# Kernel optimization log

Hardware: AMD Instinct MI355X
Metric: run time of the kernel (lower is better)

The kernel has to match this reference:

```python
import jax, jax.numpy as jnp
import numpy as np

LN_EPS = 1e-5
NRM_EPS = 1e-12


def layernorm(x, w, b):
    mu = x.mean(-1, keepdims=True)
    var = ((x - mu) ** 2).mean(-1, keepdims=True)
    return (x - mu) * jax.lax.rsqrt(var + LN_EPS) * w + b


def cdist(x, y):
    # Euclidean pairwise distance over trailing (N, C): (..., N, C) x (..., M, C) -> (..., N, M)
    x2 = (x * x).sum(-1)
    y2 = (y * y).sum(-1)
    xy = jnp.einsum('...ic,...jc->...ij', x, y)
    return jnp.sqrt(jnp.maximum(x2[..., :, None] + y2[..., None, :] - 2.0 * xy, NRM_EPS))


def l2norm_last(x):
    n = jnp.sqrt((x * x).sum(-1, keepdims=True))
    return x / jnp.maximum(n, NRM_EPS)


def attn_qcs_sd(anchor, positive, neg1, neg2, k, alpha):
    # anchor/positive: (B,N,C); neg1/neg2: (2,B,N,C)
    # torch.tensor(neg) in the original detaches neg1/neg2 from autograd
    neg1 = jax.lax.stop_gradient(neg1)
    neg2 = jax.lax.stop_gradient(neg2)
    k = k + 1.0
    S_p = cdist(positive, anchor)           # (B,N,N)
    S_p = S_p - S_p.min()
    S_p = S_p.max() - S_p
    S_a = l2norm_last(S_p).sum(1)           # (B,N)
    S_p1 = l2norm_last(jnp.swapaxes(S_p, 1, 2)).sum(1)  # (B,N)

    def proc(D):  # (B,N,N) -> (B,N)
        D = D - D.min()
        return l2norm_last(D).sum(1)

    def pair(neg, tgt):  # neg (2,B,N,C), tgt (B,N,C)
        D = cdist(neg, jnp.broadcast_to(tgt[None], neg.shape))  # (2,B,N,N)
        return proc(D[0]), proc(D[1])

    d11, d12 = pair(neg1, anchor)
    d21, d22 = pair(neg2, anchor)
    map1 = S_a + k * ((d11 + d12) / 2 * alpha + (1 - alpha) * ((d21 + d22) / 2))
    d11, d12 = pair(neg1, positive)
    d21, d22 = pair(neg2, positive)
    map2 = S_p1 + k * ((d11 + d12) / 2 * alpha + (1 - alpha) * ((d21 + d22) / 2))
    return map1[..., None], map2[..., None]  # (B,N,1) each


def setup_inputs() -> dict:
    key = jax.random.key(0)
    B, N, C = 8, 1024, 768
    ks = jax.random.split(key, 12)
    s = 1.0 / np.sqrt(C)
    sh = 1.0 / np.sqrt(4 * C)
    return {
        'anchor': jax.random.normal(ks[0], (B, N, C), jnp.float32),
        'positive': jax.random.normal(ks[1], (B, N, C), jnp.float32),
        'neg1': jax.random.normal(ks[2], (2, B, N, C), jnp.float32),
        'neg2': jax.random.normal(ks[3], (2, B, N, C), jnp.float32),
        'norm1_w': jnp.ones((C,), jnp.float32),
        'norm1_b': jnp.zeros((C,), jnp.float32),
        'norm2_w': jnp.ones((C,), jnp.float32),
        'norm2_b': jnp.zeros((C,), jnp.float32),
        'proj_W': jax.random.uniform(ks[4], (C, 2 * C), jnp.float32, -s, s),
        'proj_b': jax.random.uniform(ks[5], (2 * C,), jnp.float32, -s, s),
        'fc1_W': jax.random.uniform(ks[6], (C, 4 * C), jnp.float32, -s, s),
        'fc1_b': jax.random.uniform(ks[7], (4 * C,), jnp.float32, -s, s),
        'fc2_W': jax.random.uniform(ks[8], (4 * C, C), jnp.float32, -sh, sh),
        'fc2_b': jax.random.uniform(ks[9], (C,), jnp.float32, -sh, sh),
        'theta': jnp.float32(0.0),
        'alpha': jnp.float32(0.0),
    }


def reference(anchor, positive, neg1, neg2, norm1_w, norm1_b, norm2_w, norm2_b,
              proj_W, proj_b, fc1_W, fc1_b, fc2_W, fc2_b, theta, alpha):
    def projsplit(x):
        y = x @ proj_W + proj_b
        C = x.shape[-1]
        return y[..., :C], y[..., C:]  # qk, v

    anc = layernorm(anchor, norm1_w, norm1_b)
    pos = layernorm(positive, norm1_w, norm1_b)
    n1 = layernorm(neg1, norm1_w, norm1_b)   # (2,B,N,C)
    n2 = layernorm(neg2, norm1_w, norm1_b)
    qk_x, v_x = projsplit(anc)
    qk_p, v_p = projsplit(pos)
    qk_n1, v_n1 = projsplit(n1)
    qk_n2, v_n2 = projsplit(n2)

    k = jnp.tanh(theta)
    al = jax.nn.sigmoid(alpha)

    a_a, a_p = attn_qcs_sd(qk_x, qk_p, qk_n1, qk_n2, k, al)
    n1_a, n1_p = attn_qcs_sd(qk_n1[0], qk_n1[1], jnp.stack([qk_x, qk_p]), qk_n2, k, al)
    n2_a, n2_p = attn_qcs_sd(qk_n2[0], qk_n2[1], jnp.stack([qk_x, qk_p]), qk_n1, k, al)

    anc_o = a_a * v_x + anc
    pos_o = a_p * v_p + pos
    neg1_o = jnp.stack([n1_a * v_n1[0] * n1[0], n1_p * v_n1[1] * n1[1]])
    neg2_o = jnp.stack([n2_a * v_n2[0] * n2[0], n2_p * v_n2[1] * n2[1]])

    def block(x):
        h = layernorm(x, norm2_w, norm2_b)
        h = jax.nn.gelu(h @ fc1_W + fc1_b, approximate=False) @ fc2_W + fc2_b
        return h + x

    return block(anc_o), block(pos_o), block(neg1_o), block(neg2_o)
```

## Files before the change

kernel.cpp:

```cpp
#include <hip/hip_runtime.h>
#include <hip/hip_bf16.h>


typedef short bshort8 __attribute__((ext_vector_type(8)));
typedef unsigned short u16x8 __attribute__((ext_vector_type(8)));
typedef float f32x4  __attribute__((ext_vector_type(4)));

#define AS1 __attribute__((address_space(1)))
#define AS3 __attribute__((address_space(3)))

#define B_   8
#define N_   1024
#define C_   768
#define MT   8192
#define M6   49152

#define OFF_QKNORM   0ull
#define OFF_MAPS     196608ull
#define OFF_STATS    393216ull
#define OFF_WBUF     2359296ull
#define OFF_MM       3342336ull
#define MEMSET_BYTES 3342464ull
#define OFF_WTPROJ   3342592ull
#define OFF_WTFC1    5701888ull
#define OFF_WTFC2    10420480ull
#define OFF_LNBF     15139072ull
#define OFF_QKBF     90636544ull
#define OFF_XHBF     OFF_QKBF
#define OFF_VBF      166134016ull
#define OFF_DBUF     241631488ull
#define OFF_H1BF     OFF_DBUF

__constant__ int cSU[15] = {1,3,5, 2,3,4,5, 2,3,4,5, 4,5,4,5};
__constant__ int cSV[15] = {0,2,4, 0,0,0,0, 1,1,1,1, 2,2,3,3};
__constant__ int cTA[15] = {0,0,0, 1,1,2,2, 1,1,2,2, 2,2,2,2};
__constant__ int cTB[15] = {0,0,0, 1,1,1,1, 1,1,1,1, 2,2,2,2};

__device__ __forceinline__ void gll16(const void* g, void* l) {
    __builtin_amdgcn_global_load_lds((const AS1 unsigned int*)g,
                                     (AS3 unsigned int*)l, 16, 0, 0);
}
__device__ __forceinline__ unsigned short f2bu(float v) {
    __hip_bfloat16 h = __float2bfloat16(v);
    return *reinterpret_cast<unsigned short*>(&h);
}
__device__ __forceinline__ float bu2f(unsigned short u) {
    __hip_bfloat16 h;
    *reinterpret_cast<unsigned short*>(&h) = u;
    return __bfloat162float(h);
}
__device__ __forceinline__ int xcd_swz(int flat, int nwg) {
    return (flat & 7) * (nwg >> 3) + (flat >> 3);
}

__device__ __forceinline__ void gemm256_core(const __hip_bfloat16* __restrict__ A,
                                             const __hip_bfloat16* __restrict__ Bt,
                                             int lda, int ldb, int kTiles,
                                             char* smem, f32x4 acc[8][4])
{
    const int tid = threadIdx.x;
    const int L   = tid & 63;
    const int m   = L & 15, q = L >> 4;
    const int w   = tid >> 6;
    const int wm  = w >> 2, wn = w & 3;

    const char* gA[4]; const char* gB[4];
    int lA[4], lB[4];
#pragma unroll
    for (int i = 0; i < 4; ++i) {
        int c  = tid + 512 * i;
        int r  = c >> 3;
        int gk = (c & 7) ^ (r & 7);
        gA[i] = (const char*)(A  + (size_t)r * lda) + gk * 16;
        gB[i] = (const char*)(Bt + (size_t)r * ldb) + gk * 16;
        lA[i] = c * 16;
        lB[i] = 32768 + c * 16;
    }
    const int aBase = wm * 16384 + m * 128;
    const int bBase = 32768 + wn * 8192 + m * 128;
    const int s0    = (q ^ (m & 7)) * 16;

    f32x4 z = {0.f, 0.f, 0.f, 0.f};
#pragma unroll
    for (int i = 0; i < 8; ++i)
#pragma unroll
        for (int j = 0; j < 4; ++j) acc[i][j] = z;

#pragma unroll
    for (int i = 0; i < 4; ++i) { gll16(gA[i], smem + lA[i]); gll16(gB[i], smem + lB[i]); }
#pragma unroll
    for (int i = 0; i < 4; ++i) {
        gll16(gA[i] + 128, smem + 65536 + lA[i]);
        gll16(gB[i] + 128, smem + 65536 + lB[i]);
    }

    for (int kt = 0; kt < kTiles; ++kt) {
        if (kt + 1 < kTiles) asm volatile("s_waitcnt vmcnt(8)" ::: "memory");
        else                 asm volatile("s_waitcnt vmcnt(0)" ::: "memory");
        __builtin_amdgcn_s_barrier();
        char* cur = smem + (kt & 1) * 65536;

        bshort8 af0[8], bf0[4], af1[8], bf1[4];
        const int so0 = s0, so1 = s0 ^ 64;
#pragma unroll
        for (int mi = 0; mi < 8; ++mi)
            af0[mi] = *(const bshort8*)(cur + aBase + mi * 2048 + so0);
#pragma unroll
        for (int nj = 0; nj < 4; ++nj)
            bf0[nj] = *(const bshort8*)(cur + bBase + nj * 2048 + so0);
#pragma unroll
        for (int mi = 0; mi < 8; ++mi)
            af1[mi] = *(const bshort8*)(cur + aBase + mi * 2048 + so1);
#pragma unroll
        for (int nj = 0; nj < 4; ++nj)
            bf1[nj] = *(const bshort8*)(cur + bBase + nj * 2048 + so1);

        asm volatile("s_waitcnt lgkmcnt(0)" ::: "memory");
        __builtin_amdgcn_s_barrier();

        if (kt + 2 < kTiles) {
            const int adv = (kt + 2) * 128;
#pragma unroll
            for (int i = 0; i < 4; ++i) {
                gll16(gA[i] + adv, cur + lA[i]);
                gll16(gB[i] + adv, cur + lB[i]);
            }
        }

        __builtin_amdgcn_s_setprio(1);
#pragma unroll
        for (int mi = 0; mi < 8; ++mi)
#pragma unroll
            for (int nj = 0; nj < 4; ++nj)
                acc[mi][nj] = __builtin_amdgcn_mfma_f32_16x16x32_bf16(af0[mi], bf0[nj], acc[mi][nj], 0, 0, 0);
#pragma unroll
        for (int mi = 0; mi < 8; ++mi)
#pragma unroll
            for (int nj = 0; nj < 4; ++nj)
                acc[mi][nj] = __builtin_amdgcn_mfma_f32_16x16x32_bf16(af1[mi], bf1[nj], acc[mi][nj], 0, 0, 0);
        __builtin_amdgcn_s_setprio(0);
    }
}

__global__ __launch_bounds__(256) void transpose_conv(const float* __restrict__ in,
                                                      __hip_bfloat16* __restrict__ out,
                                                      int R, int C)
{
    __shared__ float tile[32][33];
    int bx = blockIdx.x * 32, by = blockIdx.y * 32;
    int tx = threadIdx.x, ty = threadIdx.y;
#pragma unroll
    for (int i = 0; i < 32; i += 8)
        tile[ty + i][tx] = in[(size_t)(by + ty + i) * C + bx + tx];
    __syncthreads();
#pragma unroll
    for (int i = 0; i < 32; i += 8)
        out[(size_t)(bx + ty + i) * R + by + tx] = __float2bfloat16(tile[tx][ty + i]);
}

__global__ void init_mm(unsigned int* mm)
{
    int i = threadIdx.x;
    if (i < 15) { mm[i] = 0x7f800000u; mm[15 + i] = 0u; }
}

__global__ __launch_bounds__(256) void ln1_kernel(const float* __restrict__ anchor,
                                                  const float* __restrict__ positive,
                                                  const float* __restrict__ neg1,
                                                  const float* __restrict__ neg2,
                                                  const float* __restrict__ w1,
                                                  const float* __restrict__ b1,
                                                  __hip_bfloat16* __restrict__ lnbf)
{
    int w = threadIdx.x >> 6, L = threadIdx.x & 63;
    int r = blockIdx.x * 4 + w;
    int t = r >> 13, within = r & 8191;
    const float* src;
    if      (t == 0) src = anchor   + (size_t)within * C_;
    else if (t == 1) src = positive + (size_t)within * C_;
    else if (t <  4) src = neg1 + ((size_t)(t - 2) * MT + within) * C_;
    else             src = neg2 + ((size_t)(t - 4) * MT + within) * C_;
    float4 x[3]; float s = 0.f, sq = 0.f;
#pragma unroll
    for (int j = 0; j < 3; ++j) {
        x[j] = *(const float4*)(src + 4 * L + 256 * j);
        s  += x[j].x + x[j].y + x[j].z + x[j].w;
        sq += x[j].x*x[j].x + x[j].y*x[j].y + x[j].z*x[j].z + x[j].w*x[j].w;
    }
#pragma unroll
    for (int o = 1; o < 64; o <<= 1) { s += __shfl_xor(s, o, 64); sq += __shfl_xor(sq, o, 64); }
    float mu  = s * (1.f / 768.f);
    float var = sq * (1.f / 768.f) - mu * mu;
    float rs  = rsqrtf(var + 1e-5f);
    __hip_bfloat16* dst = lnbf + (size_t)r * C_;
#pragma unroll
    for (int j = 0; j < 3; ++j) {
        int c = 4 * L + 256 * j;
        float4 wv = *(const float4*)(w1 + c);
        float4 bv = *(const float4*)(b1 + c);
        ushort4 o;
        o.x = f2bu((x[j].x - mu) * rs * wv.x + bv.x);
        o.y = f2bu((x[j].y - mu) * rs * wv.y + bv.y);
        o.z = f2bu((x[j].z - mu) * rs * wv.z + bv.z);
        o.w = f2bu((x[j].w - mu) * rs * wv.w + bv.w);
        *(ushort4*)(dst + c) = o;
    }
}

__global__ __launch_bounds__(512, 2) void gemm_proj(const __hip_bfloat16* __restrict__ A,
                                                    const __hip_bfloat16* __restrict__ Wt,
                                                    const float* __restrict__ bias,
                                                    __hip_bfloat16* __restrict__ qkbf,
                                                    __hip_bfloat16* __restrict__ vbf,
                                                    float* __restrict__ qknorm)
{
    __shared__ __align__(16) char smem[131072];
    int flat = blockIdx.x + 6 * blockIdx.y;
    int sf   = xcd_swz(flat, 6 * 192);
    int bx = sf % 6, by = sf / 6;
    f32x4 acc[8][4];
    gemm256_core(A + (size_t)by * 256 * C_, Wt + (size_t)bx * 256 * C_,
                 C_, C_, 12, smem, acc);
    int tid = threadIdx.x, w = tid >> 6, L = tid & 63, m = L & 15, q = L >> 4;
    int wm = w >> 2, wn = w & 3;
    int rowBase = by * 256 + wm * 128;
    int colBase = bx * 256 + wn * 64;
    bool isQK = (bx < 3);
    float bv[4];
#pragma unroll
    for (int nj = 0; nj < 4; ++nj) bv[nj] = bias[colBase + nj * 16 + m];
#pragma unroll
    for (int mi = 0; mi < 8; ++mi) {
#pragma unroll
        for (int r = 0; r < 4; ++r) {
            int row = rowBase + mi * 16 + 4 * q + r;
            float sqsum = 0.f;
#pragma unroll
            for (int nj = 0; nj < 4; ++nj) {
                int col = colBase + nj * 16 + m;
                float val = acc[mi][nj][r] + bv[nj];
                if (isQK) {
                    qkbf[(size_t)row * C_ + col] = __float2bfloat16(val);
                    sqsum += val * val;
                } else {
                    vbf[(size_t)row * C_ + (col - C_)] = __float2bfloat16(val);
                }
            }
            if (isQK) {
#pragma unroll
                for (int o = 1; o < 16; o <<= 1) sqsum += __shfl_xor(sqsum, o, 64);
                if (m == 0) atomicAdd(qknorm + row, sqsum);
            }
        }
    }
}

__global__ __launch_bounds__(512, 2) void gram_kernel(const __hip_bfloat16* __restrict__ qkbf,
                                                      const float* __restrict__ qknorm,
                                                      __hip_bfloat16* __restrict__ Dbuf,
                                                      float* __restrict__ stats,
                                                      unsigned int* __restrict__ mm,
                                                      int sb)
{
    __shared__ __align__(16) char smem[131072];
    int flat = blockIdx.x + 16 * blockIdx.y + 128 * blockIdx.z;
    int nwg  = 128 * gridDim.z;
    int sf   = xcd_swz(flat, nwg);
    int tile = sf & 15;
    int b    = (sf >> 4) & 7;
    int z    = sf >> 7;
    int slab = sb + z;
    int TI = tile >> 2, TJ = tile & 3;
    int u = cSU[slab], v = cSV[slab];

    const __hip_bfloat16* Ab = qkbf + (size_t)(u * MT + b * N_ + TI * 256) * C_;
    const __hip_bfloat16* Bb = qkbf + (size_t)(v * MT + b * N_ + TJ * 256) * C_;
    f32x4 acc[8][4];
    gemm256_core(Ab, Bb, C_, C_, 12, smem, acc);

    int tid = threadIdx.x, w = tid >> 6, L = tid & 63, m = L & 15, q = L >> 4;
    int wm = w >> 2, wn = w & 3;
    int rowBase = TI * 256 + wm * 128;
    int colBase = TJ * 256 + wn * 64;
    const float* nu = qknorm + u * MT + b * N_;
    const float* nv = qknorm + v * MT + b * N_;
    float nbv[4];
#pragma unroll
    for (int nj = 0; nj < 4; ++nj) nbv[nj] = nv[colBase + nj * 16 + m];

    unsigned short* Dz = (unsigned short*)Dbuf + (size_t)z * 8388608ull + ((size_t)b << 20);
    int tile128 = (TI * 2 + wm) * 8 + TJ * 2 + (wn >> 1);
    float* rs1 = stats + (size_t)slab * 32768;
    float* rs2 = rs1 + 8192;
    float* cs1 = rs1 + 16384;
    float* cs2 = rs1 + 24576;

    float dmin = 3.0e38f, dmax = 0.f;
    float col1[4] = {0.f,0.f,0.f,0.f}, col2[4] = {0.f,0.f,0.f,0.f};
#pragma unroll
    for (int mi = 0; mi < 8; ++mi) {
        float na[4];
#pragma unroll
        for (int r = 0; r < 4; ++r) na[r] = nu[rowBase + mi * 16 + 4 * q + r];
        float dv[4][4];
        float h1v[4] = {0.f,0.f,0.f,0.f}, h2v[4] = {0.f,0.f,0.f,0.f};
#pragma unroll
        for (int nj = 0; nj < 4; ++nj) {
#pragma unroll
            for (int r = 0; r < 4; ++r) {
                float d = sqrtf(fmaxf(na[r] + nbv[nj] - 2.f * acc[mi][nj][r], 1e-12f));
                dv[nj][r] = d;
                h1v[r] += d; h2v[r] += d * d;
                col1[nj] += d; col2[nj] += d * d;
                dmin = fminf(dmin, d); dmax = fmaxf(dmax, d);
            }
        }
        unsigned short* base = Dz + (size_t)tile128 * 16384
                             + (((mi >> 2) << 1) | (wn & 1)) * 4096
                             + ((mi & 3) * 2) * 512 + m * 32 + q * 8;
#pragma unroll
        for (int tp = 0; tp < 2; ++tp) {
            u16x8 pk;
#pragma unroll
            for (int e = 0; e < 8; ++e)
                pk[e] = f2bu(dv[2 * tp + (e >> 2)][e & 3]);
            *(u16x8*)(base + tp * 512) = pk;
        }
#pragma unroll
        for (int r = 0; r < 4; ++r) {
            float h1 = h1v[r], h2 = h2v[r];
#pragma unroll
            for (int o = 1; o < 16; o <<= 1) { h1 += __shfl_xor(h1, o, 64); h2 += __shfl_xor(h2, o, 64); }
            if (m == 0) {
                int row = rowBase + mi * 16 + 4 * q + r;
                atomicAdd(rs1 + b * N_ + row, h1);
                atomicAdd(rs2 + b * N_ + row, h2);
            }
        }
    }
#pragma unroll
    for (int nj = 0; nj < 4; ++nj) {
        float c1 = col1[nj], c2 = col2[nj];
        c1 += __shfl_xor(c1, 16, 64); c1 += __shfl_xor(c1, 32, 64);
        c2 += __shfl_xor(c2, 16, 64); c2 += __shfl_xor(c2, 32, 64);
        if (q == 0) {
            int col = colBase + nj * 16 + m;
            atomicAdd(cs1 + b * N_ + col, c1);
            atomicAdd(cs2 + b * N_ + col, c2);
        }
    }
#pragma unroll
    for (int o = 1; o < 64; o <<= 1) {
        dmin = fminf(dmin, __shfl_xor(dmin, o, 64));
        dmax = fmaxf(dmax, __shfl_xor(dmax, o, 64));
    }
    if (L == 0) {
        atomicMin(mm + slab, __float_as_uint(dmin));
        atomicMax(mm + 15 + slab, __float_as_uint(dmax));
    }
}

__global__ __launch_bounds__(256) void weights_kernel(const float* __restrict__ stats,
                                                      const unsigned int* __restrict__ mm,
                                                      float* __restrict__ wbuf,
                                                      float* __restrict__ maps,
                                                      const float* __restrict__ theta,
                                                      const float* __restrict__ alpha,
                                                      int sb)
{
    int job = blockIdx.x, b = blockIdx.y;
    int slab = sb + (job >> 1);
    int useB = job & 1;
    const float* s1 = stats + (size_t)slab * 32768 + useB * 16384;
    const float* s2 = s1 + 8192;
    int type = useB ? cTB[slab] : cTA[slab];
    int dst  = useB ? cSU[slab] : cSV[slab];
    float off = (type == 0) ? __uint_as_float(mm[15 + slab]) : __uint_as_float(mm[slab]);
    float k  = tanhf(theta[0]) + 1.0f;
    float al = 1.0f / (1.0f + expf(-alpha[0]));
    float cf = (type == 0) ? -1.0f : ((type == 1) ? 0.5f * k * al : 0.5f * k * (1.0f - al));
    float* wout = wbuf + (size_t)slab * 16384 + useB * 8192 + b * N_;

    float sumw = 0.f;
    for (int i = threadIdx.x; i < N_; i += 256) {
        float a1 = s1[b * N_ + i], a2 = s2[b * N_ + i];
        float nrm2  = fmaxf(a2 - 2.f * off * a1 + (float)N_ * off * off, 0.f);
        float denom = fmaxf(sqrtf(nrm2), 1e-12f);
        float wv = cf / denom;
        wout[i] = wv;
        sumw += wv;
    }
    int w = threadIdx.x >> 6, L = threadIdx.x & 63;
#pragma unroll
    for (int o = 1; o < 64; o <<= 1) sumw += __shfl_xor(sumw, o, 64);
    __shared__ float red[4];
    if (L == 0) red[w] = sumw;
    __syncthreads();
    float tot = red[0] + red[1] + red[2] + red[3];
    float Cb = -off * tot;
    for (int j = threadIdx.x; j < N_; j += 256)
        atomicAdd(maps + (size_t)dst * MT + b * N_ + j, Cb);
}

__global__ __launch_bounds__(256) void wsum_kernel(const __hip_bfloat16* __restrict__ Dbuf,
                                                   const float* __restrict__ wbuf,
                                                   float* __restrict__ maps,
                                                   int sb)
{
    int z = blockIdx.z, slab = sb + z, b = blockIdx.y;
    int tile = blockIdx.x;
    int ti = tile >> 3, tj = tile & 7;
    int u = cSU[slab], v = cSV[slab];
    int tid = threadIdx.x, w = tid >> 6, L = tid & 63, m = L & 15, q = L >> 4;
    const unsigned short* Dc = (const unsigned short*)Dbuf + (size_t)z * 8388608ull
                               + ((size_t)b << 20) + (size_t)tile * 16384 + w * 4096;
    const float* wr = wbuf + (size_t)slab * 16384 + b * N_ + ti * 128;
    const float* wc = wbuf + (size_t)slab * 16384 + 8192 + b * N_ + tj * 128;

    __shared__ float swr[128], swc[128];
    if (threadIdx.x < 128) swr[threadIdx.x] = wr[threadIdx.x];
    else                   swc[threadIdx.x - 128] = wc[threadIdx.x - 128];
    __syncthreads();

    int wrbase = (w >> 1) * 64, wcbase = (w & 1) * 64;
    float wc1[4];
#pragma unroll
    for (int t = 0; t < 4; ++t) wc1[t] = swc[wcbase + 16 * t + m];
    float wr4[4][4];
#pragma unroll
    for (int s = 0; s < 4; ++s)
#pragma unroll
        for (int r = 0; r < 4; ++r) wr4[s][r] = swr[wrbase + 16 * s + 4 * q + r];

    float rowacc[4][4];
#pragma unroll
    for (int s = 0; s < 4; ++s)
#pragma unroll
        for (int r = 0; r < 4; ++r) rowacc[s][r] = 0.f;
    float colacc[4] = {0.f,0.f,0.f,0.f};

#pragma unroll
    for (int s = 0; s < 4; ++s) {
#pragma unroll
        for (int tp = 0; tp < 2; ++tp) {
            u16x8 d8 = *(const u16x8*)(Dc + (s * 2 + tp) * 512 + m * 32 + q * 8);
#pragma unroll
            for (int e = 0; e < 8; ++e) {
                int t = 2 * tp + (e >> 2), r = e & 3;
                float d = bu2f(d8[e]);
                rowacc[s][r] += wc1[t] * d;
                colacc[t]    += wr4[s][r] * d;
            }
        }
    }
#pragma unroll
    for (int s = 0; s < 4; ++s)
#pragma unroll
        for (int r = 0; r < 4; ++r) {
            float h = rowacc[s][r];
#pragma unroll
            for (int o = 1; o < 16; o <<= 1) h += __shfl_xor(h, o, 64);
            if (m == 0)
                atomicAdd(maps + (size_t)u * MT + b * N_ + ti * 128 + wrbase + 16 * s + 4 * q + r, h);
        }
#pragma unroll
    for (int t = 0; t < 4; ++t) {
        float c = colacc[t];
        c += __shfl_xor(c, 16, 64); c += __shfl_xor(c, 32, 64);
        if (q == 0)
            atomicAdd(maps + (size_t)v * MT + b * N_ + tj * 128 + wcbase + 16 * t + m, c);
    }
}

__global__ __launch_bounds__(256) void combine_ln2(const float* __restrict__ maps,
                                                   const __hip_bfloat16* __restrict__ vbf,
                                                   const __hip_bfloat16* __restrict__ lnbf,
                                                   const float* __restrict__ w2,
                                                   const float* __restrict__ b2,
                                                   float* __restrict__ dout,
                                                   __hip_bfloat16* __restrict__ xhbf)
{
    int w = threadIdx.x >> 6, L = threadIdx.x & 63;
    int r = blockIdx.x * 4 + w;
    int t = r >> 13;
    float mv = maps[r];
    const __hip_bfloat16* vp = vbf + (size_t)r * C_;
    const __hip_bfloat16* lp = lnbf + (size_t)r * C_;
    float x[12]; float s = 0.f, sq = 0.f;
#pragma unroll
    for (int j = 0; j < 3; ++j) {
        int c = 4 * L + 256 * j;
        ushort4 vv = *(const ushort4*)(vp + c);
        ushort4 ll = *(const ushort4*)(lp + c);
        float xv[4];
        xv[0] = (t < 2) ? (mv * bu2f(vv.x) + bu2f(ll.x)) : (mv * bu2f(vv.x) * bu2f(ll.x));
        xv[1] = (t < 2) ? (mv * bu2f(vv.y) + bu2f(ll.y)) : (mv * bu2f(vv.y) * bu2f(ll.y));
        xv[2] = (t < 2) ? (mv * bu2f(vv.z) + bu2f(ll.z)) : (mv * bu2f(vv.z) * bu2f(ll.z));
        xv[3] = (t < 2) ? (mv * bu2f(vv.w) + bu2f(ll.w)) : (mv * bu2f(vv.w) * bu2f(ll.w));
        float4 xo = {xv[0], xv[1], xv[2], xv[3]};
        *(float4*)(dout + (size_t)r * C_ + c) = xo;
#pragma unroll
        for (int e = 0; e < 4; ++e) { x[4*j+e] = xv[e]; s += xv[e]; sq += xv[e]*xv[e]; }
    }
#pragma unroll
    for (int o = 1; o < 64; o <<= 1) { s += __shfl_xor(s, o, 64); sq += __shfl_xor(sq, o, 64); }
    float mu  = s * (1.f / 768.f);
    float var = sq * (1.f / 768.f) - mu * mu;
    float rs  = rsqrtf(var + 1e-5f);
    __hip_bfloat16* dst = xhbf + (size_t)r * C_;
#pragma unroll
    for (int j = 0; j < 3; ++j) {
        int c = 4 * L + 256 * j;
        float4 wv = *(const float4*)(w2 + c);
        float4 bv = *(const float4*)(b2 + c);
        ushort4 o;
        o.x = f2bu((x[4*j+0] - mu) * rs * wv.x + bv.x);
        o.y = f2bu((x[4*j+1] - mu) * rs * wv.y + bv.y);
        o.z = f2bu((x[4*j+2] - mu) * rs * wv.z + bv.z);
        o.w = f2bu((x[4*j+3] - mu) * rs * wv.w + bv.w);
        *(ushort4*)(dst + c) = o;
    }
}

__global__ __launch_bounds__(512, 2) void gemm_ffn1(const __hip_bfloat16* __restrict__ A,
                                                    const __hip_bfloat16* __restrict__ Wt,
                                                    const float* __restrict__ bias,
                                                    __hip_bfloat16* __restrict__ h1)
{
    __shared__ __align__(16) char smem[131072];
    int flat = blockIdx.x + 12 * blockIdx.y;
    int sf   = xcd_swz(flat, 12 * 96);
    int bx = sf % 12, by = sf / 12;
    f32x4 acc[8][4];
    gemm256_core(A + (size_t)by * 256 * C_, Wt + (size_t)bx * 256 * C_,
                 C_, C_, 12, smem, acc);
    int tid = threadIdx.x, w = tid >> 6, L = tid & 63, m = L & 15, q = L >> 4;
    int wm = w >> 2, wn = w & 3;
    int rowBase = by * 256 + wm * 128;
    int colBase = bx * 256 + wn * 64;
    float bv[4];
#pragma unroll
    for (int nj = 0; nj < 4; ++nj) bv[nj] = bias[colBase + nj * 16 + m];
#pragma unroll
    for (int mi = 0; mi < 8; ++mi)
#pragma unroll
        for (int r = 0; r < 4; ++r) {
            int row = rowBase + mi * 16 + 4 * q + r;
#pragma unroll
            for (int nj = 0; nj < 4; ++nj) {
                int col = colBase + nj * 16 + m;
                float val = acc[mi][nj][r] + bv[nj];
                float ge  = 0.5f * val * (1.0f + erff(val * 0.70710678118654752f));
                h1[(size_t)row * 3072 + col] = __float2bfloat16(ge);
            }
        }
}

__global__ __launch_bounds__(512, 2) void gemm_ffn2(const __hip_bfloat16* __restrict__ A,
                                                    const __hip_bfloat16* __restrict__ Wt,
                                                    const float* __restrict__ bias,
                                                    float* __restrict__ out)
{
    __shared__ __align__(16) char smem[131072];
    int flat = blockIdx.x + 3 * blockIdx.y;
    int sf   = xcd_swz(flat, 3 * 96);
    int bx = sf % 3, by = sf / 3;
    f32x4 acc[8][4];
    gemm256_core(A + (size_t)by * 256 * 3072, Wt + (size_t)bx * 256 * 3072,
                 3072, 3072, 48, smem, acc);
    int tid = threadIdx.x, w = tid >> 6, L = tid & 63, m = L & 15, q = L >> 4;
    int wm = w >> 2, wn = w & 3;
    int rowBase = by * 256 + wm * 128;
    int colBase = bx * 256 + wn * 64;
    float bv[4];
#pragma unroll
    for (int nj = 0; nj < 4; ++nj) bv[nj] = bias[colBase + nj * 16 + m];
#pragma unroll
    for (int mi = 0; mi < 8; ++mi)
#pragma unroll
        for (int r = 0; r < 4; ++r) {
            int row = rowBase + mi * 16 + 4 * q + r;
#pragma unroll
            for (int nj = 0; nj < 4; ++nj) {
                int col = colBase + nj * 16 + m;
                size_t idx = (size_t)row * C_ + col;
                out[idx] = out[idx] + acc[mi][nj][r] + bv[nj];
            }
        }
}

extern "C" void kernel_launch(void* const* d_in, const int* in_sizes, int n_in,
                              void* d_out, int out_size, void* d_ws, size_t ws_size,
                              hipStream_t stream)
{
    (void)in_sizes; (void)n_in; (void)out_size; (void)ws_size;
    const float* anchor   = (const float*)d_in[0];
    const float* positive = (const float*)d_in[1];
    const float* neg1     = (const float*)d_in[2];
    const float* neg2     = (const float*)d_in[3];
    const float* n1w      = (const float*)d_in[4];
    const float* n1b      = (const float*)d_in[5];
    const float* n2w      = (const float*)d_in[6];
    const float* n2b      = (const float*)d_in[7];
    const float* projW    = (const float*)d_in[8];
    const float* projb    = (const float*)d_in[9];
    const float* fc1W     = (const float*)d_in[10];
    const float* fc1b     = (const float*)d_in[11];
    const float* fc2W     = (const float*)d_in[12];
    const float* fc2b     = (const float*)d_in[13];
    const float* theta    = (const float*)d_in[14];
    const float* alpha    = (const float*)d_in[15];
    float* dout = (float*)d_out;

    char* ws = (char*)d_ws;
    float*          qknorm = (float*)(ws + OFF_QKNORM);
    float*          maps   = (float*)(ws + OFF_MAPS);
    float*          stats  = (float*)(ws + OFF_STATS);
    float*          wbuf   = (float*)(ws + OFF_WBUF);
    unsigned int*   mm     = (unsigned int*)(ws + OFF_MM);
    __hip_bfloat16* WtProj = (__hip_bfloat16*)(ws + OFF_WTPROJ);
    __hip_bfloat16* WtFc1  = (__hip_bfloat16*)(ws + OFF_WTFC1);
    __hip_bfloat16* WtFc2  = (__hip_bfloat16*)(ws + OFF_WTFC2);
    __hip_bfloat16* lnbf   = (__hip_bfloat16*)(ws + OFF_LNBF);
    __hip_bfloat16* qkbf   = (__hip_bfloat16*)(ws + OFF_QKBF);
    __hip_bfloat16* xhbf   = (__hip_bfloat16*)(ws + OFF_XHBF);
    __hip_bfloat16* vbf    = (__hip_bfloat16*)(ws + OFF_VBF);
    __hip_bfloat16* Dbuf   = (__hip_bfloat16*)(ws + OFF_DBUF);
    __hip_bfloat16* h1bf   = (__hip_bfloat16*)(ws + OFF_H1BF);

    hipMemsetAsync(ws, 0, MEMSET_BYTES, stream);
    init_mm<<<1, 64, 0, stream>>>(mm);

    transpose_conv<<<dim3(48, 24), dim3(32, 8), 0, stream>>>(projW, WtProj, 768, 1536);
    transpose_conv<<<dim3(96, 24), dim3(32, 8), 0, stream>>>(fc1W,  WtFc1,  768, 3072);
    transpose_conv<<<dim3(24, 96), dim3(32, 8), 0, stream>>>(fc2W,  WtFc2,  3072, 768);

    ln1_kernel<<<12288, 256, 0, stream>>>(anchor, positive, neg1, neg2, n1w, n1b, lnbf);

    gemm_proj<<<dim3(6, 192), 512, 0, stream>>>(lnbf, WtProj, projb, qkbf, vbf, qknorm);

    for (int g = 0; g < 2; ++g) {
        int sb = g * 8;
        int ns = g ? 7 : 8;
        gram_kernel<<<dim3(16, 8, ns), 512, 0, stream>>>(qkbf, qknorm, Dbuf, stats, mm, sb);
        weights_kernel<<<dim3(2 * ns, 8), 256, 0, stream>>>(stats, mm, wbuf, maps, theta, alpha, sb);
        wsum_kernel<<<dim3(64, 8, ns), 256, 0, stream>>>(Dbuf, wbuf, maps, sb);
    }

    combine_ln2<<<12288, 256, 0, stream>>>(maps, vbf, lnbf, n2w, n2b, dout, xhbf);

    for (int ch = 0; ch < 2; ++ch) {
        size_t ro = (size_t)ch * 24576;
        gemm_ffn1<<<dim3(12, 96), 512, 0, stream>>>(xhbf + ro * C_, WtFc1, fc1b, h1bf);
        gemm_ffn2<<<dim3(3, 96), 512, 0, stream>>>(h1bf, WtFc2, fc2b, dout + ro * C_);
    }
}
```

Baseline: 1.747 ms.

## Split GEMM k-tile into four quadrant phases interleaving LDS reads with MFMA

Restructures the inner loop of the 256x256 bf16 GEMM core. It no longer loads all A/B fragments and then runs 64 MFMAs. It now processes the 8x4 accumulator block in four quadrants, loading only the fragments each quadrant needs, with barriers and priority bumps between phases. The aim is to overlap LDS reads with matrix-core work across waves and to cut register pressure from holding all fragments at once. The cost is extra barriers per k-tile, and the global prefetch is issued later in the iteration.

```diff
diff --git a/kernel.cpp b/kernel.cpp
--- a/kernel.cpp
+++ b/kernel.cpp
@@ -53,6 +53,10 @@
     return (flat & 7) * (nwg >> 3) + (flat >> 3);
 }
 
+#define SBAR()  asm volatile("s_barrier" ::: "memory")
+#define WVM(N)  asm volatile("s_waitcnt vmcnt(" #N ")" ::: "memory")
+#define WLG0()  asm volatile("s_waitcnt lgkmcnt(0)" ::: "memory")
+
 __device__ __forceinline__ void gemm256_core(const __hip_bfloat16* __restrict__ A,
                                              const __hip_bfloat16* __restrict__ Bt,
                                              int lda, int ldb, int kTiles,
@@ -79,6 +83,7 @@
     const int aBase = wm * 16384 + m * 128;
     const int bBase = 32768 + wn * 8192 + m * 128;
     const int s0    = (q ^ (m & 7)) * 16;
+    const int s1    = s0 ^ 64;
 
     f32x4 z = {0.f, 0.f, 0.f, 0.f};
 #pragma unroll
@@ -95,28 +100,68 @@
     }
 
     for (int kt = 0; kt < kTiles; ++kt) {
-        if (kt + 1 < kTiles) asm volatile("s_waitcnt vmcnt(8)" ::: "memory");
-        else                 asm volatile("s_waitcnt vmcnt(0)" ::: "memory");
-        __builtin_amdgcn_s_barrier();
+        if (kt + 1 < kTiles) { WVM(8); }
+        else                 { WVM(0); }
+        SBAR();
         char* cur = smem + (kt & 1) * 65536;
 
-        bshort8 af0[8], bf0[4], af1[8], bf1[4];
-        const int so0 = s0, so1 = s0 ^ 64;
-#pragma unroll
-        for (int mi = 0; mi < 8; ++mi)
-            af0[mi] = *(const bshort8*)(cur + aBase + mi * 2048 + so0);
-#pragma unroll
-        for (int nj = 0; nj < 4; ++nj)
-            bf0[nj] = *(const bshort8*)(cur + bBase + nj * 2048 + so0);
-#pragma unroll
-        for (int mi = 0; mi < 8; ++mi)
-            af1[mi] = *(const bshort8*)(cur + aBase + mi * 2048 + so1);
-#pragma unroll
-        for (int nj = 0; nj < 4; ++nj)
-            bf1[nj] = *(const bshort8*)(cur + bBase + nj * 2048 + so1);
-
-        asm volatile("s_waitcnt lgkmcnt(0)" ::: "memory");
-        __builtin_amdgcn_s_barrier();
+        bshort8 af[4][2], bf0[2][2], bf1[2][2];
+
+#pragma unroll
+        for (int i = 0; i < 4; ++i) {
+            af[i][0] = *(const bshort8*)(cur + aBase + i * 2048 + s0);
+            af[i][1] = *(const bshort8*)(cur + aBase + i * 2048 + s1);
+        }
+#pragma unroll
+        for (int j = 0; j < 2; ++j) {
+            bf0[j][0] = *(const bshort8*)(cur + bBase + j * 2048 + s0);
+            bf0[j][1] = *(const bshort8*)(cur + bBase + j * 2048 + s1);
+        }
+        SBAR(); WLG0();
+        __builtin_amdgcn_s_setprio(1);
+#pragma unroll
+        for (int ks = 0; ks < 2; ++ks)
+#pragma unroll
+            for (int i = 0; i < 4; ++i)
+#pragma unroll
+                for (int j = 0; j < 2; ++j)
+                    acc[i][j] = __builtin_amdgcn_mfma_f32_16x16x32_bf16(af[i][ks], bf0[j][ks], acc[i][j], 0, 0, 0);
+        __builtin_amdgcn_s_setprio(0);
+        SBAR();
+
+#pragma unroll
+        for (int j = 0; j < 2; ++j) {
+            bf1[j][0] = *(const bshort8*)(cur + bBase + (2 + j) * 2048 + s0);
+            bf1[j][1] = *(const bshort8*)(cur + bBase + (2 + j) * 2048 + s1);
+        }
+        SBAR(); WLG0();
+        __builtin_amdgcn_s_setprio(1);
+#pragma unroll
+        for (int ks = 0; ks < 2; ++ks)
+#pragma unroll
+            for (int i = 0; i < 4; ++i)
+#pragma unroll
+                for (int j = 0; j < 2; ++j)
+                    acc[i][2 + j] = __builtin_amdgcn_mfma_f32_16x16x32_bf16(af[i][ks], bf1[j][ks], acc[i][2 + j], 0, 0, 0);
+        __builtin_amdgcn_s_setprio(0);
+        SBAR();
+
+#pragma unroll
+        for (int i = 0; i < 4; ++i) {
+            af[i][0] = *(const bshort8*)(cur + aBase + (4 + i) * 2048 + s0);
+            af[i][1] = *(const bshort8*)(cur + aBase + (4 + i) * 2048 + s1);
+        }
+        SBAR(); WLG0();
+        __builtin_amdgcn_s_setprio(1);
+#pragma unroll
+        for (int ks = 0; ks < 2; ++ks)
+#pragma unroll
+            for (int i = 0; i < 4; ++i)
+#pragma unroll
+                for (int j = 0; j < 2; ++j)
+                    acc[4 + i][j] = __builtin_amdgcn_mfma_f32_16x16x32_bf16(af[i][ks], bf0[j][ks], acc[4 + i][j], 0, 0, 0);
+        __builtin_amdgcn_s_setprio(0);
+        SBAR();
 
         if (kt + 2 < kTiles) {
             const int adv = (kt + 2) * 128;
@@ -126,18 +171,14 @@
                 gll16(gB[i] + adv, cur + lB[i]);
             }
         }
-
         __builtin_amdgcn_s_setprio(1);
 #pragma unroll
-        for (int mi = 0; mi < 8; ++mi)
-#pragma unroll
-            for (int nj = 0; nj < 4; ++nj)
-                acc[mi][nj] = __builtin_amdgcn_mfma_f32_16x16x32_bf16(af0[mi], bf0[nj], acc[mi][nj], 0, 0, 0);
-#pragma unroll
-        for (int mi = 0; mi < 8; ++mi)
-#pragma unroll
-            for (int nj = 0; nj < 4; ++nj)
-                acc[mi][nj] = __builtin_amdgcn_mfma_f32_16x16x32_bf16(af1[mi], bf1[nj], acc[mi][nj], 0, 0, 0);
+        for (int ks = 0; ks < 2; ++ks)
+#pragma unroll
+            for (int i = 0; i < 4; ++i)
+#pragma unroll
+                for (int j = 0; j < 2; ++j)
+                    acc[4 + i][2 + j] = __builtin_amdgcn_mfma_f32_16x16x32_bf16(af[i][ks], bf1[j][ks], acc[4 + i][2 + j], 0, 0, 0);
         __builtin_amdgcn_s_setprio(0);
     }
 }
```

After: 1.824 ms. +4.4%, slower.
